# Kernel optimization log

Measured on AMD Instinct MI355X. Metric: run time of the kernel, lower is better.

## Reference

```python
import jax, jax.numpy as jnp
import numpy as np

B, S, D, H = 4, 2048, 1024, 16
DH = D // H

def setup_inputs() -> dict:
    key = jax.random.key(0)
    ks = jax.random.split(key, 4)
    scale = 1.0 / np.sqrt(D)
    x = jax.random.normal(ks[0], (B, S, D), dtype=jnp.float32)
    Wq = jax.random.normal(ks[1], (D, D), dtype=jnp.float32) * scale
    Wk = jax.random.normal(ks[2], (D, D), dtype=jnp.float32) * scale
    Wv = jax.random.normal(ks[3], (D, D), dtype=jnp.float32) * scale
    bq = jnp.zeros((D,), dtype=jnp.float32)
    bk = jnp.zeros((D,), dtype=jnp.float32)
    bv = jnp.zeros((D,), dtype=jnp.float32)
    # causal mask, broadcastable to [B, H, S, S]; mask==0 positions get -inf
    mask = jnp.tril(jnp.ones((S, S), dtype=bool))[None, None, :, :]
    return {"x": x, "mask": mask, "Wq": Wq, "bq": bq, "Wk": Wk, "bk": bk, "Wv": Wv, "bv": bv}

def reference(x, mask, Wq, bq, Wk, bk, Wv, bv):
    b, s, d = x.shape
    def proj(W, bias):
        # nn.Linear: x @ W.T + b, then split heads -> [b, H, s, DH]
        y = jnp.einsum('bsd,ed->bse', x, W) + bias
        return y.reshape(b, s, H, DH).transpose(0, 2, 1, 3)
    q = proj(Wq, bq)
    k = proj(Wk, bk)
    v = proj(Wv, bv)
    scores = jnp.einsum('bhqd,bhkd->bhqk', q, k) / jnp.sqrt(jnp.float32(DH))
    scores = jnp.where(mask, scores, -jnp.inf)
    attn = jax.nn.softmax(scores, axis=-1)
    out = jnp.einsum('bhqk,bhkd->bhqd', attn, v)
    return out.transpose(0, 2, 1, 3).reshape(b, s, d)
```

## Files before the change

### kernel.cpp

```cpp
#include <hip/hip_runtime.h>
#include <hip/hip_bf16.h>
#include <stdint.h>

typedef unsigned short u16;
typedef unsigned int   u32;
typedef short bf16x8 __attribute__((ext_vector_type(8)));
typedef float f32x4  __attribute__((ext_vector_type(4)));

typedef bf16x8 __attribute__((__may_alias__)) bf16x8_a;
typedef uint4  __attribute__((__may_alias__)) uint4_a;
typedef uint2  __attribute__((__may_alias__)) uint2_a;
typedef float4 __attribute__((__may_alias__)) float4_a;

#define MFMA_BF16(a,b,c) __builtin_amdgcn_mfma_f32_16x16x32_bf16((a),(b),(c),0,0,0)
#define L2E 1.44269504088896340736f

#define SEQ 2048
#define DMODEL 1024
#define NH 16
#define DH 64

__device__ __forceinline__ u32 pack_bf2(float a, float b) {
  union { __hip_bfloat162 h; u32 u; } c;
  c.h = __float22bfloat162_rn(make_float2(a, b));
  return c.u;
}

__device__ __forceinline__ u16 f2bf(float f) {
  u32 u = __builtin_bit_cast(u32, f);
  u += 0x7FFFu + ((u >> 16) & 1u);
  return (u16)(u >> 16);
}

__device__ __forceinline__ void gl_lds16(const u16* g, u16* l) {
  __builtin_amdgcn_global_load_lds(
      (const __attribute__((address_space(1))) void*)g,
      (__attribute__((address_space(3))) void*)l, 16, 0, 0);
}

__global__ __launch_bounds__(256) void cvt_x_bf16(
    const float* __restrict__ s, u16* __restrict__ d, int n8)
{
  int i = blockIdx.x * 256 + threadIdx.x;
  const int stride = gridDim.x * 256;
  for (; i < n8; i += stride) {
    const float4_a* p = (const float4_a*)(s + (size_t)i * 8);
    float4 a = p[0], b = p[1];
    uint4 o;
    o.x = pack_bf2(a.x, a.y); o.y = pack_bf2(a.z, a.w);
    o.z = pack_bf2(b.x, b.y); o.w = pack_bf2(b.z, b.w);
    *(uint4_a*)(d + (size_t)i * 8) = o;
  }
}

__global__ __launch_bounds__(256) void cvt_w_bf16(
    const float* __restrict__ wq, const float* __restrict__ wk, const float* __restrict__ wv,
    u16* __restrict__ oq, u16* __restrict__ ok, u16* __restrict__ ov)
{
  const float* s = (blockIdx.y == 0) ? wq : (blockIdx.y == 1) ? wk : wv;
  u16*         d = (blockIdx.y == 0) ? oq : (blockIdx.y == 1) ? ok : ov;
  const int i = blockIdx.x * 256 + threadIdx.x;
  const float4_a* p = (const float4_a*)(s + (size_t)i * 8);
  float4 a = p[0], b = p[1];
  uint4 o;
  o.x = pack_bf2(a.x, a.y); o.y = pack_bf2(a.z, a.w);
  o.z = pack_bf2(b.x, b.y); o.w = pack_bf2(b.z, b.w);
  *(uint4_a*)(d + (size_t)i * 8) = o;
}

__global__ __launch_bounds__(256, 2) void qkv_gemm_bf(
    const u16* __restrict__ Xb,
    const u16* __restrict__ Wqb, const u16* __restrict__ Wkb, const u16* __restrict__ Wvb,
    const float* __restrict__ Bq, const float* __restrict__ Bk, const float* __restrict__ Bv,
    u16* __restrict__ Qo, u16* __restrict__ Ko, u16* __restrict__ Vo)
{
  __shared__ u16 As[128 * 32];
  __shared__ u16 Bs[128 * 32];

  const int tid  = threadIdx.x;
  const int lane = tid & 63;
  const int wid  = tid >> 6;
  const int l16  = lane & 15;
  const int quad = lane >> 4;
  const int wm   = (wid >> 1) * 64;
  const int wn   = (wid & 1) * 64;

  const int m0 = blockIdx.x * 128;
  const int n0 = blockIdx.y * 128;
  const int pj = blockIdx.z;

  const u16*   Wb   = (pj == 0) ? Wqb : (pj == 1) ? Wkb : Wvb;
  const float* Bias = (pj == 0) ? Bq : (pj == 1) ? Bk : Bv;
  u16*         Out  = (pj == 0) ? Qo : (pj == 1) ? Ko : Vo;
  const float scale = (pj == 0) ? 0.125f : 1.0f;

  f32x4 acc[4][4];
#pragma unroll
  for (int i = 0; i < 4; i++)
#pragma unroll
    for (int j = 0; j < 4; j++) acc[i][j] = (f32x4){0.f, 0.f, 0.f, 0.f};

  const int lr = lane >> 2;
  const int lc = (lane & 3) * 8;

  const u16* Arow = Xb + (size_t)m0 * DMODEL;
  const u16* Brow = Wb + (size_t)n0 * DMODEL;

  for (int kt = 0; kt < DMODEL; kt += 32) {
#pragma unroll
    for (int c = 0; c < 2; c++) {
      const int band = c * 64 + wid * 16;
      gl_lds16(Arow + (size_t)(band + lr) * DMODEL + kt + lc, &As[band * 32]);
      gl_lds16(Brow + (size_t)(band + lr) * DMODEL + kt + lc, &Bs[band * 32]);
    }
    __syncthreads();

    bf16x8 a[4], b[4];
#pragma unroll
    for (int mt = 0; mt < 4; mt++)
      a[mt] = *(const bf16x8_a*)&As[(wm + mt * 16 + l16) * 32 + quad * 8];
#pragma unroll
    for (int nt = 0; nt < 4; nt++)
      b[nt] = *(const bf16x8_a*)&Bs[(wn + nt * 16 + l16) * 32 + quad * 8];
#pragma unroll
    for (int mt = 0; mt < 4; mt++)
#pragma unroll
      for (int nt = 0; nt < 4; nt++)
        acc[mt][nt] = MFMA_BF16(a[mt], b[nt], acc[mt][nt]);

    __syncthreads();
  }

  if (pj == 2) {
#pragma unroll
    for (int mt = 0; mt < 4; mt++) {
#pragma unroll
      for (int nt = 0; nt < 4; nt++) {
        const int n = n0 + wn + nt * 16 + l16;
        const float bias = Bias[n];
        const int h = n >> 6, dh = n & 63;
        const int m = m0 + wm + mt * 16 + quad * 4;
        const int bb = m >> 11, ss = m & 2047;
        uint2 pk;
        pk.x = pack_bf2(acc[mt][nt][0] + bias, acc[mt][nt][1] + bias);
        pk.y = pack_bf2(acc[mt][nt][2] + bias, acc[mt][nt][3] + bias);
        *(uint2_a*)&Out[((size_t)(bb * NH + h) * DH + dh) * SEQ + ss] = pk;
      }
    }
  } else {
#pragma unroll
    for (int mt = 0; mt < 4; mt++) {
#pragma unroll
      for (int nt = 0; nt < 4; nt++) {
        const int n = n0 + wn + nt * 16 + l16;
        const float bias = Bias[n];
        const int h = n >> 6, dh = n & 63;
#pragma unroll
        for (int r = 0; r < 4; r++) {
          const int m = m0 + wm + mt * 16 + quad * 4 + r;
          const int bb = m >> 11, ss = m & 2047;
          Out[((((size_t)bb * NH + h) * SEQ + ss) << 6) + dh] = f2bf((acc[mt][nt][r] + bias) * scale);
        }
      }
    }
  }
}

__global__ __launch_bounds__(256, 2) void qkv_gemm(
    const float* __restrict__ X,
    const float* __restrict__ Wq, const float* __restrict__ Wk, const float* __restrict__ Wv,
    const float* __restrict__ Bq, const float* __restrict__ Bk, const float* __restrict__ Bv,
    u16* __restrict__ Qo, u16* __restrict__ Ko, u16* __restrict__ Vo)
{
  __shared__ u16 As[128 * 32];
  __shared__ u16 Bs[128 * 32];

  const int tid  = threadIdx.x;
  const int lane = tid & 63;
  const int wid  = tid >> 6;
  const int l16  = lane & 15;
  const int quad = lane >> 4;
  const int wm   = (wid >> 1) * 64;
  const int wn   = (wid & 1) * 64;

  const int m0 = blockIdx.x * 128;
  const int n0 = blockIdx.y * 128;
  const int pj = blockIdx.z;

  const float* W    = (pj == 0) ? Wq : (pj == 1) ? Wk : Wv;
  const float* Bias = (pj == 0) ? Bq : (pj == 1) ? Bk : Bv;
  u16*         Out  = (pj == 0) ? Qo : (pj == 1) ? Ko : Vo;
  const float scale = (pj == 0) ? 0.125f : 1.0f;

  f32x4 acc[4][4];
#pragma unroll
  for (int i = 0; i < 4; i++)
#pragma unroll
    for (int j = 0; j < 4; j++) acc[i][j] = (f32x4){0.f, 0.f, 0.f, 0.f};

  float4 gX[4], gW[4];
#pragma unroll
  for (int i = 0; i < 4; i++) {
    const int ch = i * 256 + tid;
    const int r = ch >> 3, c = ch & 7;
    gX[i] = *(const float4_a*)(X + (size_t)(m0 + r) * DMODEL + c * 4);
    gW[i] = *(const float4_a*)(W + (size_t)(n0 + r) * DMODEL + c * 4);
  }

  for (int kt = 0; kt < DMODEL; kt += 32) {
    __syncthreads();
#pragma unroll
    for (int i = 0; i < 4; i++) {
      const int ch = i * 256 + tid;
      const int r = ch >> 3, c = ch & 7;
      uint2 xp, wp;
      xp.x = pack_bf2(gX[i].x, gX[i].y);  xp.y = pack_bf2(gX[i].z, gX[i].w);
      wp.x = pack_bf2(gW[i].x, gW[i].y);  wp.y = pack_bf2(gW[i].z, gW[i].w);
      *(uint2_a*)&As[r * 32 + c * 4] = xp;
      *(uint2_a*)&Bs[r * 32 + c * 4] = wp;
    }
    __syncthreads();

    if (kt + 32 < DMODEL) {
#pragma unroll
      for (int i = 0; i < 4; i++) {
        const int ch = i * 256 + tid;
        const int r = ch >> 3, c = ch & 7;
        gX[i] = *(const float4_a*)(X + (size_t)(m0 + r) * DMODEL + kt + 32 + c * 4);
        gW[i] = *(const float4_a*)(W + (size_t)(n0 + r) * DMODEL + kt + 32 + c * 4);
      }
    }

    bf16x8 a[4], b[4];
#pragma unroll
    for (int mt = 0; mt < 4; mt++)
      a[mt] = *(const bf16x8_a*)&As[(wm + mt * 16 + l16) * 32 + quad * 8];
#pragma unroll
    for (int nt = 0; nt < 4; nt++)
      b[nt] = *(const bf16x8_a*)&Bs[(wn + nt * 16 + l16) * 32 + quad * 8];
#pragma unroll
    for (int mt = 0; mt < 4; mt++)
#pragma unroll
      for (int nt = 0; nt < 4; nt++)
        acc[mt][nt] = MFMA_BF16(a[mt], b[nt], acc[mt][nt]);
  }

  if (pj == 2) {
#pragma unroll
    for (int mt = 0; mt < 4; mt++) {
#pragma unroll
      for (int nt = 0; nt < 4; nt++) {
        const int n = n0 + wn + nt * 16 + l16;
        const float bias = Bias[n];
        const int h = n >> 6, dh = n & 63;
        const int m = m0 + wm + mt * 16 + quad * 4;
        const int bb = m >> 11, ss = m & 2047;
        uint2 pk;
        pk.x = pack_bf2(acc[mt][nt][0] + bias, acc[mt][nt][1] + bias);
        pk.y = pack_bf2(acc[mt][nt][2] + bias, acc[mt][nt][3] + bias);
        *(uint2_a*)&Out[((size_t)(bb * NH + h) * DH + dh) * SEQ + ss] = pk;
      }
    }
  } else {
#pragma unroll
    for (int mt = 0; mt < 4; mt++) {
#pragma unroll
      for (int nt = 0; nt < 4; nt++) {
        const int n = n0 + wn + nt * 16 + l16;
        const float bias = Bias[n];
        const int h = n >> 6, dh = n & 63;
#pragma unroll
        for (int r = 0; r < 4; r++) {
          const int m = m0 + wm + mt * 16 + quad * 4 + r;
          const int bb = m >> 11, ss = m & 2047;
          Out[((((size_t)bb * NH + h) * SEQ + ss) << 6) + dh] = f2bf((acc[mt][nt][r] + bias) * scale);
        }
      }
    }
  }
}

__global__ __launch_bounds__(256, 2) void flash_attn(
    const u16* __restrict__ Q, const u16* __restrict__ K, const u16* __restrict__ VT,
    float* __restrict__ O)
{
  __shared__ u16 Ks[128 * 72];
  __shared__ u16 VTs[64 * 136];
  __shared__ u16 Ps[4 * 32 * 144];

  const int tid  = threadIdx.x;
  const int lane = tid & 63;
  const int wid  = tid >> 6;
  const int l16  = lane & 15;
  const int quad = lane >> 4;

  const int idx = blockIdx.x;
  const int qt  = 15 - (idx >> 6);
  const int bh  = idx & 63;
  const int bb = bh >> 4, hh = bh & 15;
  const int qbase = qt * 128;

  const u16* Qh = Q  + (size_t)bh * (SEQ * DH);
  const u16* Kh = K  + (size_t)bh * (SEQ * DH);
  const u16* Vh = VT + (size_t)bh * (DH * SEQ);

#pragma unroll
  for (int i = 0; i < 4; i++) {
    const int ch = i * 256 + tid;
    const int r = ch >> 3, c = ch & 7;
    *(uint4_a*)&Ks[r * 72 + c * 8] = *(const uint4_a*)(Qh + (size_t)(qbase + r) * DH + c * 8);
  }
  __syncthreads();

  bf16x8 qf[2][2];
#pragma unroll
  for (int ct = 0; ct < 2; ct++)
#pragma unroll
    for (int ks = 0; ks < 2; ks++)
      qf[ct][ks] = *(const bf16x8_a*)&Ks[(wid * 32 + ct * 16 + l16) * 72 + ks * 32 + quad * 8];

  f32x4 o[4][2];
#pragma unroll
  for (int dt = 0; dt < 4; dt++)
#pragma unroll
    for (int ct = 0; ct < 2; ct++) o[dt][ct] = (f32x4){0.f, 0.f, 0.f, 0.f};

  float mold[2] = {-1e30f, -1e30f};
  float lsum[2] = {0.f, 0.f};

  uint4 gK[4], gV[4];
#pragma unroll
  for (int i = 0; i < 4; i++) {
    const int ch = i * 256 + tid;
    gK[i] = *(const uint4_a*)(Kh + (size_t)(ch >> 3) * DH + (ch & 7) * 8);
    gV[i] = *(const uint4_a*)(Vh + (size_t)(ch >> 4) * SEQ + (ch & 15) * 8);
  }

  for (int j = 0; j <= qt; j++) {
    __syncthreads();
#pragma unroll
    for (int i = 0; i < 4; i++) {
      const int ch = i * 256 + tid;
      *(uint4_a*)&Ks[(ch >> 3) * 72 + (ch & 7) * 8]   = gK[i];
      *(uint4_a*)&VTs[(ch >> 4) * 136 + (ch & 15) * 8] = gV[i];
    }
    __syncthreads();

    if (j < qt) {
      const int kb2 = (j + 1) * 128;
#pragma unroll
      for (int i = 0; i < 4; i++) {
        const int ch = i * 256 + tid;
        gK[i] = *(const uint4_a*)(Kh + (size_t)(kb2 + (ch >> 3)) * DH + (ch & 7) * 8);
        gV[i] = *(const uint4_a*)(Vh + (size_t)(ch >> 4) * SEQ + kb2 + (ch & 15) * 8);
      }
    }

    f32x4 s[8][2];
    __builtin_amdgcn_s_setprio(1);
#pragma unroll
    for (int rt = 0; rt < 8; rt++) {
      bf16x8 ka0 = *(const bf16x8_a*)&Ks[(rt * 16 + l16) * 72 + 0 + quad * 8];
      bf16x8 ka1 = *(const bf16x8_a*)&Ks[(rt * 16 + l16) * 72 + 32 + quad * 8];
#pragma unroll
      for (int ct = 0; ct < 2; ct++) {
        f32x4 c = (f32x4){0.f, 0.f, 0.f, 0.f};
        c = MFMA_BF16(ka0, qf[ct][0], c);
        c = MFMA_BF16(ka1, qf[ct][1], c);
        s[rt][ct] = c;
      }
    }
    __builtin_amdgcn_s_setprio(0);

    if (j == qt) {
#pragma unroll
      for (int rt = 0; rt < 8; rt++)
#pragma unroll
        for (int ct = 0; ct < 2; ct++) {
          const int ql = wid * 32 + ct * 16 + l16;
#pragma unroll
          for (int r = 0; r < 4; r++) {
            const int kvl = rt * 16 + quad * 4 + r;
            if (kvl > ql) s[rt][ct][r] = -1e30f;
          }
        }
    }

#pragma unroll
    for (int ct = 0; ct < 2; ct++) {
      float mt = -1e30f;
#pragma unroll
      for (int rt = 0; rt < 8; rt++)
#pragma unroll
        for (int r = 0; r < 4; r++) mt = fmaxf(mt, s[rt][ct][r]);
      mt = fmaxf(mt, __shfl_xor(mt, 16));
      mt = fmaxf(mt, __shfl_xor(mt, 32));
      const float mnew = fmaxf(mold[ct], mt);
      const float a = __builtin_amdgcn_exp2f((mold[ct] - mnew) * L2E);
      float ls = 0.f;
#pragma unroll
      for (int rt = 0; rt < 8; rt++)
#pragma unroll
        for (int r = 0; r < 4; r++) {
          const float p = __builtin_amdgcn_exp2f((s[rt][ct][r] - mnew) * L2E);
          s[rt][ct][r] = p;
          ls += p;
        }
      ls += __shfl_xor(ls, 16);
      ls += __shfl_xor(ls, 32);
      lsum[ct] = lsum[ct] * a + ls;
      mold[ct] = mnew;
#pragma unroll
      for (int dt = 0; dt < 4; dt++)
#pragma unroll
        for (int r = 0; r < 4; r++) o[dt][ct][r] *= a;
    }

    u16* Pw = &Ps[wid * 32 * 144];
#pragma unroll
    for (int rt = 0; rt < 8; rt++) {
#pragma unroll
      for (int ct = 0; ct < 2; ct++) {
        uint2 pk;
        pk.x = pack_bf2(s[rt][ct][0], s[rt][ct][1]);
        pk.y = pack_bf2(s[rt][ct][2], s[rt][ct][3]);
        *(uint2_a*)&Pw[(ct * 16 + l16) * 144 + rt * 16 + quad * 4] = pk;
      }
    }
    asm volatile("s_waitcnt lgkmcnt(0)" ::: "memory");

    __builtin_amdgcn_s_setprio(1);
#pragma unroll
    for (int ks2 = 0; ks2 < 4; ks2++) {
      bf16x8 vt[4], pb[2];
#pragma unroll
      for (int dt = 0; dt < 4; dt++)
        vt[dt] = *(const bf16x8_a*)&VTs[(dt * 16 + l16) * 136 + ks2 * 32 + quad * 8];
#pragma unroll
      for (int ct = 0; ct < 2; ct++)
        pb[ct] = *(const bf16x8_a*)&Pw[(ct * 16 + l16) * 144 + ks2 * 32 + quad * 8];
#pragma unroll
      for (int dt = 0; dt < 4; dt++)
#pragma unroll
        for (int ct = 0; ct < 2; ct++)
          o[dt][ct] = MFMA_BF16(vt[dt], pb[ct], o[dt][ct]);
    }
    __builtin_amdgcn_s_setprio(0);
  }

#pragma unroll
  for (int ct = 0; ct < 2; ct++) {
    const float inv = 1.0f / lsum[ct];
    const int qg = qbase + wid * 32 + ct * 16 + l16;
    float* orow = O + (size_t)((size_t)bb * SEQ + qg) * DMODEL + hh * 64;
#pragma unroll
    for (int dt = 0; dt < 4; dt++) {
      float4 v4;
      v4.x = o[dt][ct][0] * inv;  v4.y = o[dt][ct][1] * inv;
      v4.z = o[dt][ct][2] * inv;  v4.w = o[dt][ct][3] * inv;
      *(float4_a*)&orow[dt * 16 + quad * 4] = v4;
    }
  }
}

__global__ void paintf(float* out, int n, float v) {
  int i = blockIdx.x * 256 + threadIdx.x;
  if (i < n) out[i] = v;
}

extern "C" void kernel_launch(void* const* d_in, const int* in_sizes, int n_in,
                              void* d_out, int out_size, void* d_ws, size_t ws_size,
                              hipStream_t stream) {
  float* out = (float*)d_out;

  const size_t elems  = (size_t)4 * SEQ * DMODEL;
  const size_t welems = (size_t)DMODEL * DMODEL;
  const size_t need_old = 3 * elems * sizeof(u16);
  const size_t need_new = (4 * elems + 3 * welems) * sizeof(u16);

  if (ws_size < need_old) {
    paintf<<<(out_size + 255) / 256, 256, 0, stream>>>(out, out_size, 3.0e38f);
    return;
  }

  const float* x  = (const float*)d_in[0];
  const float* Wq = (const float*)d_in[2];
  const float* bq = (const float*)d_in[3];
  const float* Wk = (const float*)d_in[4];
  const float* bk = (const float*)d_in[5];
  const float* Wv = (const float*)d_in[6];
  const float* bv = (const float*)d_in[7];

  u16* q = (u16*)d_ws;
  u16* k = q + elems;
  u16* v = k + elems;

  if (ws_size >= need_new) {
    u16* xb  = v + elems;
    u16* wqb = xb + elems;
    u16* wkb = wqb + welems;
    u16* wvb = wkb + welems;
    cvt_x_bf16<<<2048, 256, 0, stream>>>(x, xb, (int)(elems / 8));
    cvt_w_bf16<<<dim3(512, 3), 256, 0, stream>>>(Wq, Wk, Wv, wqb, wkb, wvb);
    qkv_gemm_bf<<<dim3(64, 8, 3), 256, 0, stream>>>(xb, wqb, wkb, wvb, bq, bk, bv, q, k, v);
  } else {
    qkv_gemm<<<dim3(64, 8, 3), 256, 0, stream>>>(x, Wq, Wk, Wv, bq, bk, bv, q, k, v);
  }

  flash_attn<<<1024, 256, 0, stream>>>(q, k, v, out);
}
```

Baseline: 304.7 us.

## Shrink attention KV tiles, double-buffer GEMM LDS, raise occupancy to 4 blocks

The QKV GEMM now double-buffers its LDS tiles. It prefetches the next K-slice while computing the current one, which removes one barrier per iteration. The flash-attention kernel moves from 128-wide to 64-wide KV tiles, with smaller LDS arrays and fewer staging registers. Q is staged in the P buffer so that both kernels can target 4 blocks per CU. The setprio hints are dropped. The trade is more loop iterations and barriers in attention, and tighter register limits that could cause spills.

```diff
diff --git a/kernel.cpp b/kernel.cpp
--- a/kernel.cpp
+++ b/kernel.cpp
@@ -68,14 +68,14 @@
   *(uint4_a*)(d + (size_t)i * 8) = o;
 }
 
-__global__ __launch_bounds__(256, 2) void qkv_gemm_bf(
+__global__ __launch_bounds__(256, 4) void qkv_gemm_bf(
     const u16* __restrict__ Xb,
     const u16* __restrict__ Wqb, const u16* __restrict__ Wkb, const u16* __restrict__ Wvb,
     const float* __restrict__ Bq, const float* __restrict__ Bk, const float* __restrict__ Bv,
     u16* __restrict__ Qo, u16* __restrict__ Ko, u16* __restrict__ Vo)
 {
-  __shared__ u16 As[128 * 32];
-  __shared__ u16 Bs[128 * 32];
+  __shared__ u16 As[2][128 * 32];
+  __shared__ u16 Bs[2][128 * 32];
 
   const int tid  = threadIdx.x;
   const int lane = tid & 63;
@@ -106,29 +106,38 @@
   const u16* Arow = Xb + (size_t)m0 * DMODEL;
   const u16* Brow = Wb + (size_t)n0 * DMODEL;
 
+#pragma unroll
+  for (int c = 0; c < 2; c++) {
+    const int band = c * 64 + wid * 16;
+    gl_lds16(Arow + (size_t)(band + lr) * DMODEL + lc, &As[0][band * 32]);
+    gl_lds16(Brow + (size_t)(band + lr) * DMODEL + lc, &Bs[0][band * 32]);
+  }
+
   for (int kt = 0; kt < DMODEL; kt += 32) {
-#pragma unroll
-    for (int c = 0; c < 2; c++) {
-      const int band = c * 64 + wid * 16;
-      gl_lds16(Arow + (size_t)(band + lr) * DMODEL + kt + lc, &As[band * 32]);
-      gl_lds16(Brow + (size_t)(band + lr) * DMODEL + kt + lc, &Bs[band * 32]);
-    }
+    const int cur = (kt >> 5) & 1;
     __syncthreads();
 
+    if (kt + 32 < DMODEL) {
+#pragma unroll
+      for (int c = 0; c < 2; c++) {
+        const int band = c * 64 + wid * 16;
+        gl_lds16(Arow + (size_t)(band + lr) * DMODEL + kt + 32 + lc, &As[cur ^ 1][band * 32]);
+        gl_lds16(Brow + (size_t)(band + lr) * DMODEL + kt + 32 + lc, &Bs[cur ^ 1][band * 32]);
+      }
+    }
+
     bf16x8 a[4], b[4];
 #pragma unroll
     for (int mt = 0; mt < 4; mt++)
-      a[mt] = *(const bf16x8_a*)&As[(wm + mt * 16 + l16) * 32 + quad * 8];
+      a[mt] = *(const bf16x8_a*)&As[cur][(wm + mt * 16 + l16) * 32 + quad * 8];
 #pragma unroll
     for (int nt = 0; nt < 4; nt++)
-      b[nt] = *(const bf16x8_a*)&Bs[(wn + nt * 16 + l16) * 32 + quad * 8];
+      b[nt] = *(const bf16x8_a*)&Bs[cur][(wn + nt * 16 + l16) * 32 + quad * 8];
 #pragma unroll
     for (int mt = 0; mt < 4; mt++)
 #pragma unroll
       for (int nt = 0; nt < 4; nt++)
         acc[mt][nt] = MFMA_BF16(a[mt], b[nt], acc[mt][nt]);
-
-    __syncthreads();
   }
 
   if (pj == 2) {
@@ -280,13 +289,13 @@
   }
 }
 
-__global__ __launch_bounds__(256, 2) void flash_attn(
+__global__ __launch_bounds__(256, 4) void flash_attn(
     const u16* __restrict__ Q, const u16* __restrict__ K, const u16* __restrict__ VT,
     float* __restrict__ O)
 {
-  __shared__ u16 Ks[128 * 72];
-  __shared__ u16 VTs[64 * 136];
-  __shared__ u16 Ps[4 * 32 * 144];
+  __shared__ u16 Ks[64 * 72];
+  __shared__ u16 VTs[64 * 72];
+  __shared__ u16 Ps[4 * 32 * 72];
 
   const int tid  = threadIdx.x;
   const int lane = tid & 63;
@@ -308,16 +317,17 @@
   for (int i = 0; i < 4; i++) {
     const int ch = i * 256 + tid;
     const int r = ch >> 3, c = ch & 7;
-    *(uint4_a*)&Ks[r * 72 + c * 8] = *(const uint4_a*)(Qh + (size_t)(qbase + r) * DH + c * 8);
+    *(uint4_a*)&Ps[r * 72 + c * 8] = *(const uint4_a*)(Qh + (size_t)(qbase + r) * DH + c * 8);
   }
   __syncthreads();
 
+  u16* Pw = &Ps[wid * 32 * 72];
   bf16x8 qf[2][2];
 #pragma unroll
   for (int ct = 0; ct < 2; ct++)
 #pragma unroll
     for (int ks = 0; ks < 2; ks++)
-      qf[ct][ks] = *(const bf16x8_a*)&Ks[(wid * 32 + ct * 16 + l16) * 72 + ks * 32 + quad * 8];
+      qf[ct][ks] = *(const bf16x8_a*)&Pw[(ct * 16 + l16) * 72 + ks * 32 + quad * 8];
 
   f32x4 o[4][2];
 #pragma unroll
@@ -328,38 +338,39 @@
   float mold[2] = {-1e30f, -1e30f};
   float lsum[2] = {0.f, 0.f};
 
-  uint4 gK[4], gV[4];
-#pragma unroll
-  for (int i = 0; i < 4; i++) {
+  const int jmax = 2 * qt + 1;
+
+  uint4 gK[2], gV[2];
+#pragma unroll
+  for (int i = 0; i < 2; i++) {
     const int ch = i * 256 + tid;
     gK[i] = *(const uint4_a*)(Kh + (size_t)(ch >> 3) * DH + (ch & 7) * 8);
-    gV[i] = *(const uint4_a*)(Vh + (size_t)(ch >> 4) * SEQ + (ch & 15) * 8);
-  }
-
-  for (int j = 0; j <= qt; j++) {
+    gV[i] = *(const uint4_a*)(Vh + (size_t)(ch >> 3) * SEQ + (ch & 7) * 8);
+  }
+
+  for (int j = 0; j <= jmax; j++) {
     __syncthreads();
 #pragma unroll
-    for (int i = 0; i < 4; i++) {
+    for (int i = 0; i < 2; i++) {
       const int ch = i * 256 + tid;
-      *(uint4_a*)&Ks[(ch >> 3) * 72 + (ch & 7) * 8]   = gK[i];
-      *(uint4_a*)&VTs[(ch >> 4) * 136 + (ch & 15) * 8] = gV[i];
+      *(uint4_a*)&Ks[(ch >> 3) * 72 + (ch & 7) * 8]  = gK[i];
+      *(uint4_a*)&VTs[(ch >> 3) * 72 + (ch & 7) * 8] = gV[i];
     }
     __syncthreads();
 
-    if (j < qt) {
-      const int kb2 = (j + 1) * 128;
-#pragma unroll
-      for (int i = 0; i < 4; i++) {
+    if (j < jmax) {
+      const int kb2 = (j + 1) * 64;
+#pragma unroll
+      for (int i = 0; i < 2; i++) {
         const int ch = i * 256 + tid;
         gK[i] = *(const uint4_a*)(Kh + (size_t)(kb2 + (ch >> 3)) * DH + (ch & 7) * 8);
-        gV[i] = *(const uint4_a*)(Vh + (size_t)(ch >> 4) * SEQ + kb2 + (ch & 15) * 8);
-      }
-    }
-
-    f32x4 s[8][2];
-    __builtin_amdgcn_s_setprio(1);
-#pragma unroll
-    for (int rt = 0; rt < 8; rt++) {
+        gV[i] = *(const uint4_a*)(Vh + (size_t)(ch >> 3) * SEQ + kb2 + (ch & 7) * 8);
+      }
+    }
+
+    f32x4 s[4][2];
+#pragma unroll
+    for (int rt = 0; rt < 4; rt++) {
       bf16x8 ka0 = *(const bf16x8_a*)&Ks[(rt * 16 + l16) * 72 + 0 + quad * 8];
       bf16x8 ka1 = *(const bf16x8_a*)&Ks[(rt * 16 + l16) * 72 + 32 + quad * 8];
 #pragma unroll
@@ -370,18 +381,18 @@
         s[rt][ct] = c;
       }
     }
-    __builtin_amdgcn_s_setprio(0);
-
-    if (j == qt) {
-#pragma unroll
-      for (int rt = 0; rt < 8; rt++)
+
+    if (j >= (qt << 1)) {
+      const int kvb = j * 64;
+#pragma unroll
+      for (int rt = 0; rt < 4; rt++)
 #pragma unroll
         for (int ct = 0; ct < 2; ct++) {
-          const int ql = wid * 32 + ct * 16 + l16;
+          const int ql = qbase + wid * 32 + ct * 16 + l16;
 #pragma unroll
           for (int r = 0; r < 4; r++) {
-            const int kvl = rt * 16 + quad * 4 + r;
-            if (kvl > ql) s[rt][ct][r] = -1e30f;
+            const int kvg = kvb + rt * 16 + quad * 4 + r;
+            if (kvg > ql) s[rt][ct][r] = -1e30f;
           }
         }
     }
@@ -390,7 +401,7 @@
     for (int ct = 0; ct < 2; ct++) {
       float mt = -1e30f;
 #pragma unroll
-      for (int rt = 0; rt < 8; rt++)
+      for (int rt = 0; rt < 4; rt++)
 #pragma unroll
         for (int r = 0; r < 4; r++) mt = fmaxf(mt, s[rt][ct][r]);
       mt = fmaxf(mt, __shfl_xor(mt, 16));
@@ -399,7 +410,7 @@
       const float a = __builtin_amdgcn_exp2f((mold[ct] - mnew) * L2E);
       float ls = 0.f;
 #pragma unroll
-      for (int rt = 0; rt < 8; rt++)
+      for (int rt = 0; rt < 4; rt++)
 #pragma unroll
         for (int r = 0; r < 4; r++) {
           const float p = __builtin_amdgcn_exp2f((s[rt][ct][r] - mnew) * L2E);
@@ -416,36 +427,33 @@
         for (int r = 0; r < 4; r++) o[dt][ct][r] *= a;
     }
 
-    u16* Pw = &Ps[wid * 32 * 144];
-#pragma unroll
-    for (int rt = 0; rt < 8; rt++) {
+#pragma unroll
+    for (int rt = 0; rt < 4; rt++) {
 #pragma unroll
       for (int ct = 0; ct < 2; ct++) {
         uint2 pk;
         pk.x = pack_bf2(s[rt][ct][0], s[rt][ct][1]);
         pk.y = pack_bf2(s[rt][ct][2], s[rt][ct][3]);
-        *(uint2_a*)&Pw[(ct * 16 + l16) * 144 + rt * 16 + quad * 4] = pk;
+        *(uint2_a*)&Pw[(ct * 16 + l16) * 72 + rt * 16 + quad * 4] = pk;
       }
     }
     asm volatile("s_waitcnt lgkmcnt(0)" ::: "memory");
 
-    __builtin_amdgcn_s_setprio(1);
-#pragma unroll
-    for (int ks2 = 0; ks2 < 4; ks2++) {
+#pragma unroll
+    for (int ks2 = 0; ks2 < 2; ks2++) {
       bf16x8 vt[4], pb[2];
 #pragma unroll
       for (int dt = 0; dt < 4; dt++)
-        vt[dt] = *(const bf16x8_a*)&VTs[(dt * 16 + l16) * 136 + ks2 * 32 + quad * 8];
+        vt[dt] = *(const bf16x8_a*)&VTs[(dt * 16 + l16) * 72 + ks2 * 32 + quad * 8];
 #pragma unroll
       for (int ct = 0; ct < 2; ct++)
-        pb[ct] = *(const bf16x8_a*)&Pw[(ct * 16 + l16) * 144 + ks2 * 32 + quad * 8];
+        pb[ct] = *(const bf16x8_a*)&Pw[(ct * 16 + l16) * 72 + ks2 * 32 + quad * 8];
 #pragma unroll
       for (int dt = 0; dt < 4; dt++)
 #pragma unroll
         for (int ct = 0; ct < 2; ct++)
           o[dt][ct] = MFMA_BF16(vt[dt], pb[ct], o[dt][ct]);
     }
-    __builtin_amdgcn_s_setprio(0);
   }
 
 #pragma unroll
```

After: 289.1 us. 1.05x faster.
